# Optimization experiments

Measured on AMD Instinct MI355X. Metric: run time of the kernel, lower is better.

The kernel has to match this reference:

```python
import jax, jax.numpy as jnp
import numpy as np
from jax import lax

EPS = 1e-5

def setup_inputs() -> dict:
    key = jax.random.key(0)
    k1, k2 = jax.random.split(key)
    x = jax.random.normal(k1, (8, 256, 64, 64), dtype=jnp.float32)
    W = jax.random.normal(k2, (128, 256, 5, 5), dtype=jnp.float32) * 0.02
    gamma = jnp.ones((128,), dtype=jnp.float32)
    beta = jnp.zeros((128,), dtype=jnp.float32)
    return {"x": x, "W": W, "gamma": gamma, "beta": beta}

def reference(x, W, gamma, beta):
    B, C, H, Wd = x.shape
    # bilinear x2 upsample, half-pixel centers (== torch align_corners=False)
    up = jax.image.resize(x, (B, C, 2 * H, 2 * Wd), method="bilinear")
    # conv2d, stride 1, padding 2, no bias (norm == 'BN')
    out = lax.conv_general_dilated(
        up, W, window_strides=(1, 1), padding=[(2, 2), (2, 2)],
        dimension_numbers=("NCHW", "OIHW", "NCHW"))
    # BatchNorm2d (batch statistics, training-style refresh)
    mean = jnp.mean(out, axis=(0, 2, 3))
    var = jnp.var(out, axis=(0, 2, 3))
    inv = gamma / jnp.sqrt(var + EPS)
    out = (out - mean[None, :, None, None]) * inv[None, :, None, None] + beta[None, :, None, None]
    # activation: torch.relu
    return jax.nn.relu(out)
```

## Files before the change

### kernel.cpp

```cpp
#include <hip/hip_runtime.h>
#include <hip/hip_bf16.h>
#include <stdint.h>

typedef short s8v __attribute__((ext_vector_type(8)));
typedef float f4v __attribute__((ext_vector_type(4)));

__device__ __forceinline__ void async_copy16(const void* gsrc, void* lds_dst) {
  __builtin_amdgcn_global_load_lds(
      (const __attribute__((address_space(1))) uint32_t*)(uintptr_t)gsrc,
      (__attribute__((address_space(3))) uint32_t*)(uint32_t)(uintptr_t)lds_dst,
      16, 0, 0);
}

#define WAITVM(N) asm volatile("s_waitcnt vmcnt(" #N ")" ::: "memory")
__device__ __forceinline__ void block_barrier() {
  asm volatile("" ::: "memory");
  __builtin_amdgcn_s_barrier();
  asm volatile("" ::: "memory");
}

__global__ __launch_bounds__(256) void wpack_kernel(const float* __restrict__ W,
                                                    __hip_bfloat16* __restrict__ Wr,
                                                    float* __restrict__ gstats) {
  __shared__ __hip_bfloat16 t[256 * 26];
  const int co = blockIdx.x;
  const int tid = threadIdx.x;
  if (co == 0) gstats[tid] = 0.f;
  const float* src = W + co * 6400;
  for (int i = tid; i < 6400; i += 256) {
    int ci = i / 25;
    int pos = i - ci * 25;
    t[ci * 26 + pos] = __float2bfloat16(src[i]);
  }
  __syncthreads();
  for (int pos = 0; pos < 25; ++pos)
    Wr[pos * 32768 + co * 256 + tid] = t[tid * 26 + pos];
}

__global__ __launch_bounds__(256, 2) void upsample_kernel(const float* __restrict__ x,
                                                          __hip_bfloat16* __restrict__ up) {
  __shared__ __hip_bfloat16 lx[10 * 48 * 66];
  const int tid = threadIdx.x;
  const int bx = blockIdx.x;
  const int owb = bx & 1;
  const int ohb = (bx >> 1) & 7;
  const int cb = (bx >> 4) & 3;
  const int b = bx >> 6;
  const int oh0 = ohb * 16, ow0 = owb * 64, c0 = cb * 64;
  const int ih0 = (oh0 >> 1) - 1;
  const int iw_lo = (ow0 >> 1) - 1;
  const int aligned = (iw_lo < 0 ? 0 : iw_lo) & ~15;

  for (int i = tid; i < 64 * 10 * 12; i += 256) {
    int c = i / 120;
    int rem = i - c * 120;
    int r = rem / 12;
    int w4 = (rem - r * 12) * 4;
    int gr = ih0 + r;
    gr = gr < 0 ? 0 : (gr > 63 ? 63 : gr);
    const float4 v = *(const float4*)&x[(((b * 256 + c0 + c) * 64) + gr) * 64 + aligned + w4];
    int base = (r * 48 + w4) * 66 + c;
    lx[base]       = __float2bfloat16(v.x);
    lx[base + 66]  = __float2bfloat16(v.y);
    lx[base + 132] = __float2bfloat16(v.z);
    lx[base + 198] = __float2bfloat16(v.w);
  }
  __syncthreads();

  const int c2 = (tid & 31) * 2;
  const int owq = tid >> 5;
  uint32_t* upu = (uint32_t*)up;
  for (int it = 0; it < 128; ++it) {
    int oh_l = it >> 3;
    int ow_l = (it & 7) * 8 + owq;
    int oh = oh0 + oh_l, ow = ow0 + ow_l;
    int ihA = (oh >> 1) - ((oh & 1) ^ 1);
    float wh = (oh & 1) ? 0.75f : 0.25f;
    int iwA = (ow >> 1) - ((ow & 1) ^ 1);
    float wwt = (ow & 1) ? 0.75f : 0.25f;
    int r0 = ihA - ih0;
    int w0 = (iwA < 0 ? 0 : iwA) - aligned;
    int w1t = iwA + 1; w1t = w1t > 63 ? 63 : w1t;
    int w1 = w1t - aligned;
    uint32_t t00 = *(const uint32_t*)&lx[(r0 * 48 + w0) * 66 + c2];
    uint32_t t01 = *(const uint32_t*)&lx[(r0 * 48 + w1) * 66 + c2];
    uint32_t t10 = *(const uint32_t*)&lx[((r0 + 1) * 48 + w0) * 66 + c2];
    uint32_t t11 = *(const uint32_t*)&lx[((r0 + 1) * 48 + w1) * 66 + c2];
    float wlo = wh * wwt, wlo1 = wh * (1.f - wwt);
    float whi = (1.f - wh) * wwt, whi1 = (1.f - wh) * (1.f - wwt);
    float vlo = wlo * __uint_as_float(t00 << 16) + wlo1 * __uint_as_float(t01 << 16) +
                whi * __uint_as_float(t10 << 16) + whi1 * __uint_as_float(t11 << 16);
    float vhi = wlo * __uint_as_float(t00 & 0xffff0000u) + wlo1 * __uint_as_float(t01 & 0xffff0000u) +
                whi * __uint_as_float(t10 & 0xffff0000u) + whi1 * __uint_as_float(t11 & 0xffff0000u);
    __hip_bfloat16 h0 = __float2bfloat16(vlo);
    __hip_bfloat16 h1 = __float2bfloat16(vhi);
    uint32_t pk = (uint32_t)(*(unsigned short*)&h0) | ((uint32_t)(*(unsigned short*)&h1) << 16);
    upu[((((size_t)(b * 128 + oh) * 128) + ow) * 256 + c0 + c2) >> 1] = pk;
  }
}

#define ASLOT 8448
__global__ __launch_bounds__(512, 2) void conv_kernel(const __hip_bfloat16* __restrict__ up,
                                                      const __hip_bfloat16* __restrict__ Wr,
                                                      float* __restrict__ out,
                                                      float* __restrict__ gstats) {
  __shared__ __align__(16) unsigned short lA[5 * ASLOT];
  __shared__ __align__(16) unsigned short lB[2][128 * 64];
  __shared__ float lsum[128], lssq[128];

  const int tid = threadIdx.x;
  const int lane = tid & 63;
  const int wave = tid >> 6;
  const int wm = wave >> 1;
  const int wn = wave & 1;
  const int lane15 = lane & 15;
  const int quad = lane >> 4;
  const int wb = wave << 6;

  const int bid = blockIdx.x;
  const int orig = ((bid & 7) << 5) | (bid >> 3);
  const int b = orig >> 5;
  const int oh0 = (orig & 31) << 2;

  const f4v zero4 = {0.f, 0.f, 0.f, 0.f};
  if (tid < 128) { lsum[tid] = 0.f; lssq[tid] = 0.f; }
  if (tid < 160) {
    int s = tid >> 5, j = tid & 31;
    int rsel = j >> 3;
    int r = (rsel < 2) ? rsel : (128 + rsel);
    *(f4v*)&lA[s * ASLOT + (r * 8 + (j & 7)) * 8] = zero4;
  }

  auto stageA = [&](int slot, const __hip_bfloat16* uprow) {
#pragma unroll
    for (int t = 0; t < 2; ++t) {
      int pl = t * 512 + wb + lane;
      int riw = pl >> 3, pc = pl & 7;
      int r = riw + 2;
      int cq = pc ^ (r & 7);
      async_copy16(uprow + riw * 256 + cq * 8, (void*)&lA[slot * ASLOT + (16 + t * 512 + wb) * 8]);
    }
  };
  auto stageB = [&](const __hip_bfloat16* wsrc, int bsel) {
#pragma unroll
    for (int t = 0; t < 2; ++t) {
      int pl = t * 512 + wb + lane;
      int n = pl >> 3, pc = pl & 7;
      int cq = pc ^ (n & 7);
      async_copy16(wsrc + n * 256 + cq * 8, (void*)&lB[bsel][(t * 512 + wb) * 8]);
    }
  };

  f4v acc[8][4];
#pragma unroll
  for (int i = 0; i < 8; ++i)
#pragma unroll
    for (int j = 0; j < 4; ++j) acc[i][j] = zero4;

  for (int rr = 0; rr < 4; ++rr) {
    int ih = oh0 + rr - 2;
    if ((unsigned)ih < 128u)
      stageA(ih % 5, up + (size_t)(b * 128 + ih) * 32768);
  }
  stageB(Wr, 0);
  __syncthreads();

  int buf = 0;
  for (int cb = 0; cb < 4; ++cb) {
    const int c0 = cb << 6;
    for (int kh = 0; kh < 5; ++kh) {
      const int ih = oh0 + wm + kh - 2;
      const bool rowok = (unsigned)ih < 128u;
      const int abase = rowok ? (ih % 5) * ASLOT : 0;
      for (int kw = 0; kw < 5; ++kw) {
        const int pos = kh * 5 + kw;
        if (cb != 0 && kh == 0 && kw == 0) {
          for (int rr = 0; rr < 4; ++rr) {
            int ihn = oh0 + rr - 2;
            if ((unsigned)ihn < 128u)
              stageA(ihn % 5, up + (size_t)(b * 128 + ihn) * 32768 + c0);
          }
        }
        if (pos < 24)      stageB(Wr + (size_t)(pos + 1) * 32768 + c0, buf ^ 1);
        else if (cb < 3)   stageB(Wr + (c0 + 64), buf ^ 1);
        const bool extraA = (kw == 2) && (kh < 4) && (oh0 + kh + 2 < 128);
        if (extraA)
          stageA((oh0 + kh + 2) % 5, up + (size_t)(b * 128 + oh0 + kh + 2) * 32768 + c0);
        if (pos == 24 && cb == 3) { WAITVM(0); }
        else if (extraA)          { WAITVM(4); }
        else                      { WAITVM(2); }
        block_barrier();
        if (rowok) {
#pragma unroll
          for (int ks = 0; ks < 2; ++ks) {
            const int cq = ks * 4 + quad;
            s8v a[8], bb[4];
#pragma unroll
            for (int mt = 0; mt < 8; ++mt) {
              int r = mt * 16 + lane15 + kw;
              a[mt] = *(const s8v*)&lA[abase + (r * 8 + (cq ^ (r & 7))) * 8];
            }
#pragma unroll
            for (int nt = 0; nt < 4; ++nt) {
              int n = (wn << 6) + nt * 16 + lane15;
              bb[nt] = *(const s8v*)&lB[buf][(n * 8 + (cq ^ (n & 7))) * 8];
            }
#pragma unroll
            for (int mt = 0; mt < 8; ++mt)
#pragma unroll
              for (int nt = 0; nt < 4; ++nt)
                acc[mt][nt] = __builtin_amdgcn_mfma_f32_16x16x32_bf16(a[mt], bb[nt], acc[mt][nt], 0, 0, 0);
          }
        }
        block_barrier();
        buf ^= 1;
      }
    }
  }

  __syncthreads();
  const int oh = oh0 + wm;
#pragma unroll
  for (int nt = 0; nt < 4; ++nt) {
    const int n = (wn << 6) + nt * 16 + lane15;
    float* oc = out + ((size_t)(b * 128 + n) * 128 + oh) * 128;
    float s = 0.f, ss = 0.f;
#pragma unroll
    for (int mt = 0; mt < 8; ++mt) {
      f4v v = acc[mt][nt];
      *(f4v*)&oc[mt * 16 + (quad << 2)] = v;
      s += v.x + v.y + v.z + v.w;
      ss += v.x * v.x + v.y * v.y + v.z * v.z + v.w * v.w;
    }
    s += __shfl_xor(s, 16, 64); ss += __shfl_xor(ss, 16, 64);
    s += __shfl_xor(s, 32, 64); ss += __shfl_xor(ss, 32, 64);
    if (quad == 0) { atomicAdd(&lsum[n], s); atomicAdd(&lssq[n], ss); }
  }
  __syncthreads();
  if (tid < 128) {
    atomicAdd(&gstats[tid], lsum[tid]);
    atomicAdd(&gstats[128 + tid], lssq[tid]);
  }
}

__global__ void norm_kernel(float* __restrict__ out, const float* __restrict__ gstats,
                            const float* __restrict__ gamma, const float* __restrict__ beta) {
  __shared__ float ssb[2];
  const int c = (blockIdx.x >> 4) & 127;
  if (threadIdx.x == 0) {
    float mean = gstats[c] * (1.f / 131072.f);
    float var = gstats[128 + c] * (1.f / 131072.f) - mean * mean;
    float inv = gamma[c] * rsqrtf(var + 1e-5f);
    ssb[0] = inv;
    ssb[1] = beta[c] - mean * inv;
  }
  __syncthreads();
  int i = blockIdx.x * 256 + threadIdx.x;
  f4v v = ((f4v*)out)[i];
  float sc = ssb[0], bi = ssb[1];
  v.x = fmaxf(fmaf(v.x, sc, bi), 0.f);
  v.y = fmaxf(fmaf(v.y, sc, bi), 0.f);
  v.z = fmaxf(fmaf(v.z, sc, bi), 0.f);
  v.w = fmaxf(fmaf(v.w, sc, bi), 0.f);
  ((f4v*)out)[i] = v;
}

extern "C" void kernel_launch(void* const* d_in, const int* in_sizes, int n_in,
                              void* d_out, int out_size, void* d_ws, size_t ws_size,
                              hipStream_t stream) {
  (void)in_sizes; (void)n_in; (void)out_size; (void)ws_size;
  const float* x = (const float*)d_in[0];
  const float* W = (const float*)d_in[1];
  const float* gamma = (const float*)d_in[2];
  const float* beta = (const float*)d_in[3];
  float* out = (float*)d_out;
  char* ws = (char*)d_ws;
  __hip_bfloat16* up = (__hip_bfloat16*)ws;
  __hip_bfloat16* Wr = (__hip_bfloat16*)(ws + 67108864);
  float* gstats = (float*)(ws + 67108864 + 1638400);

  wpack_kernel<<<128, 256, 0, stream>>>(W, Wr, gstats);
  upsample_kernel<<<512, 256, 0, stream>>>(x, up);
  conv_kernel<<<256, 512, 0, stream>>>(up, Wr, out, gstats);
  norm_kernel<<<16384, 256, 0, stream>>>(out, gstats, gamma, beta);
}
```

Baseline: 306.9 us.

## Triple-buffer weight tiles to drop per-step barrier; add MFMA priority and grid-stride norm

The B (weight) tiles in LDS move from double to triple buffering. This lets the second block barrier in each kernel-position step be removed, keeping one only at channel-block boundaries. MFMA sections are wrapped in s_setprio to favour math-issuing waves. The BN+ReLU kernel becomes a grid-stride loop with fewer blocks that computes scale and bias per element instead of through shared memory. This raises LDS use and depends on waves never drifting more than one step apart, including for the A row ring.

```diff
diff --git a/kernel.cpp b/kernel.cpp
--- a/kernel.cpp
+++ b/kernel.cpp
@@ -105,7 +105,7 @@
                                                       float* __restrict__ out,
                                                       float* __restrict__ gstats) {
   __shared__ __align__(16) unsigned short lA[5 * ASLOT];
-  __shared__ __align__(16) unsigned short lB[2][128 * 64];
+  __shared__ __align__(16) unsigned short lB[3][128 * 64];
   __shared__ float lsum[128], lssq[128];
 
   const int tid = threadIdx.x;
@@ -165,7 +165,7 @@
   stageB(Wr, 0);
   __syncthreads();
 
-  int buf = 0;
+  int bcur = 0;
   for (int cb = 0; cb < 4; ++cb) {
     const int c0 = cb << 6;
     for (int kh = 0; kh < 5; ++kh) {
@@ -174,6 +174,7 @@
       const int abase = rowok ? (ih % 5) * ASLOT : 0;
       for (int kw = 0; kw < 5; ++kw) {
         const int pos = kh * 5 + kw;
+        const int bnext = (bcur == 2) ? 0 : bcur + 1;
         if (cb != 0 && kh == 0 && kw == 0) {
           for (int rr = 0; rr < 4; ++rr) {
             int ihn = oh0 + rr - 2;
@@ -181,8 +182,8 @@
               stageA(ihn % 5, up + (size_t)(b * 128 + ihn) * 32768 + c0);
           }
         }
-        if (pos < 24)      stageB(Wr + (size_t)(pos + 1) * 32768 + c0, buf ^ 1);
-        else if (cb < 3)   stageB(Wr + (c0 + 64), buf ^ 1);
+        if (pos < 24)      stageB(Wr + (size_t)(pos + 1) * 32768 + c0, bnext);
+        else if (cb < 3)   stageB(Wr + (c0 + 64), bnext);
         const bool extraA = (kw == 2) && (kh < 4) && (oh0 + kh + 2 < 128);
         if (extraA)
           stageA((oh0 + kh + 2) % 5, up + (size_t)(b * 128 + oh0 + kh + 2) * 32768 + c0);
@@ -191,6 +192,7 @@
         else                      { WAITVM(2); }
         block_barrier();
         if (rowok) {
+          __builtin_amdgcn_s_setprio(1);
 #pragma unroll
           for (int ks = 0; ks < 2; ++ks) {
             const int cq = ks * 4 + quad;
@@ -203,7 +205,7 @@
 #pragma unroll
             for (int nt = 0; nt < 4; ++nt) {
               int n = (wn << 6) + nt * 16 + lane15;
-              bb[nt] = *(const s8v*)&lB[buf][(n * 8 + (cq ^ (n & 7))) * 8];
+              bb[nt] = *(const s8v*)&lB[bcur][(n * 8 + (cq ^ (n & 7))) * 8];
             }
 #pragma unroll
             for (int mt = 0; mt < 8; ++mt)
@@ -211,14 +213,14 @@
               for (int nt = 0; nt < 4; ++nt)
                 acc[mt][nt] = __builtin_amdgcn_mfma_f32_16x16x32_bf16(a[mt], bb[nt], acc[mt][nt], 0, 0, 0);
           }
+          __builtin_amdgcn_s_setprio(0);
         }
-        block_barrier();
-        buf ^= 1;
+        if (pos == 24 && cb < 3) block_barrier();
+        bcur = bnext;
       }
     }
   }
 
-  __syncthreads();
   const int oh = oh0 + wm;
 #pragma unroll
   for (int nt = 0; nt < 4; ++nt) {
@@ -243,26 +245,23 @@
   }
 }
 
-__global__ void norm_kernel(float* __restrict__ out, const float* __restrict__ gstats,
-                            const float* __restrict__ gamma, const float* __restrict__ beta) {
-  __shared__ float ssb[2];
-  const int c = (blockIdx.x >> 4) & 127;
-  if (threadIdx.x == 0) {
+__global__ __launch_bounds__(256) void norm_kernel(float* __restrict__ out,
+                                                   const float* __restrict__ gstats,
+                                                   const float* __restrict__ gamma,
+                                                   const float* __restrict__ beta) {
+  for (int i = blockIdx.x * 256 + threadIdx.x; i < 4194304; i += 2048 * 256) {
+    f4v v = ((f4v*)out)[i];
+    int c = (i >> 12) & 127;
     float mean = gstats[c] * (1.f / 131072.f);
     float var = gstats[128 + c] * (1.f / 131072.f) - mean * mean;
-    float inv = gamma[c] * rsqrtf(var + 1e-5f);
-    ssb[0] = inv;
-    ssb[1] = beta[c] - mean * inv;
-  }
-  __syncthreads();
-  int i = blockIdx.x * 256 + threadIdx.x;
-  f4v v = ((f4v*)out)[i];
-  float sc = ssb[0], bi = ssb[1];
-  v.x = fmaxf(fmaf(v.x, sc, bi), 0.f);
-  v.y = fmaxf(fmaf(v.y, sc, bi), 0.f);
-  v.z = fmaxf(fmaf(v.z, sc, bi), 0.f);
-  v.w = fmaxf(fmaf(v.w, sc, bi), 0.f);
-  ((f4v*)out)[i] = v;
+    float sc = gamma[c] * rsqrtf(var + 1e-5f);
+    float bi = beta[c] - mean * sc;
+    v.x = fmaxf(fmaf(v.x, sc, bi), 0.f);
+    v.y = fmaxf(fmaf(v.y, sc, bi), 0.f);
+    v.z = fmaxf(fmaf(v.z, sc, bi), 0.f);
+    v.w = fmaxf(fmaf(v.w, sc, bi), 0.f);
+    ((f4v*)out)[i] = v;
+  }
 }
 
 extern "C" void kernel_launch(void* const* d_in, const int* in_sizes, int n_in,
@@ -282,5 +281,5 @@
   wpack_kernel<<<128, 256, 0, stream>>>(W, Wr, gstats);
   upsample_kernel<<<512, 256, 0, stream>>>(x, up);
   conv_kernel<<<256, 512, 0, stream>>>(up, Wr, out, gstats);
-  norm_kernel<<<16384, 256, 0, stream>>>(out, gstats, gamma, beta);
-}
+  norm_kernel<<<2048, 256, 0, stream>>>(out, gstats, gamma, beta);
+}
```

Result: faster. 297.2 us (-3.2%).
